# Optimization experiments

Hardware: AMD Instinct MI355X
Metric: run time of the kernel (lower is better)

Reference implementation:

```python
import jax, jax.numpy as jnp
import numpy as np

N_NODES = 50000
N_EDGES = 400000
IN_DIM = 128
HID_DIM = 128
OUT_DIM = 128


def setup_inputs() -> dict:
    key = jax.random.key(0)
    k_x, k_e, k_w1, k_b1, k_w2, k_b2 = jax.random.split(key, 6)
    x = jax.random.normal(k_x, (N_NODES, IN_DIM), dtype=jnp.float32)
    edge_index = jax.random.randint(k_e, (2, N_EDGES), 0, N_NODES, dtype=jnp.int64)
    # nn.Linear-style params: W is [out, in], kaiming-uniform-ish init
    lim1 = 1.0 / np.sqrt(IN_DIM)
    lim2 = 1.0 / np.sqrt(HID_DIM)
    W1 = jax.random.uniform(k_w1, (HID_DIM, IN_DIM), jnp.float32, -lim1, lim1)
    b1 = jax.random.uniform(k_b1, (HID_DIM,), jnp.float32, -lim1, lim1)
    W2 = jax.random.uniform(k_w2, (OUT_DIM, HID_DIM), jnp.float32, -lim2, lim2)
    b2 = jax.random.uniform(k_b2, (OUT_DIM,), jnp.float32, -lim2, lim2)
    return {"x": x, "edge_index": edge_index, "W1": W1, "b1": b1, "W2": W2, "b2": b2}


def reference(x, edge_index, W1, b1, W2, b2):
    # h = relu(fc1(x));  dropout in eval mode -> identity
    h = jax.nn.relu(x @ W1.T + b1)                      # [N, hid]
    src, dst = edge_index[0], edge_index[1]
    # gather messages from src, scatter-add (mean) into dst
    agg = jax.ops.segment_sum(h[src], dst, num_segments=N_NODES)      # [N, hid]
    deg = jax.ops.segment_sum(jnp.ones_like(dst, dtype=h.dtype), dst,
                              num_segments=N_NODES)                   # [N]
    deg = jnp.maximum(deg, 1.0)
    agg = agg / deg[:, None]
    # residual add + fc2
    return (agg + h) @ W2.T + b2                        # [N, out]
```

## Files before the change

kernel.cpp:

```cpp
#include <hip/hip_runtime.h>

#define N_NODES 50000
#define N_EDGES 400000
#define DIM 128
#define N_SCAN_BLK ((N_NODES + 255) / 256)
#define CNT_BLK ((N_EDGES + 1023) / 1024)
#define FC1_BLK ((N_NODES + 63) / 64)
#define AGG_BLK (N_NODES / 16)
#define PADDED_E (N_EDGES + 3 * N_NODES)

typedef unsigned short u16;
typedef unsigned int   u32;
typedef __bf16 v8bf  __attribute__((ext_vector_type(8)));
typedef float  f32x4 __attribute__((ext_vector_type(4)));
typedef u16    u16x8 __attribute__((ext_vector_type(8)));

union BF8 { u16x8 u; v8bf b; };

__device__ __forceinline__ float bf2f(u16 u) {
    union { u32 i; float f; } v; v.i = ((u32)u) << 16; return v.f;
}
__device__ __forceinline__ u16 f2bf(float f) {
    union { float f; u32 i; } v; v.f = f; u32 u = v.i;
    return (u16)((u + 0x7FFFu + ((u >> 16) & 1u)) >> 16);
}

__global__ __launch_bounds__(256, 3) void count_cast_fc1_kernel(
    const int* __restrict__ esrc, const int* __restrict__ edst,
    int* __restrict__ counts, int* __restrict__ occ,
    const float* __restrict__ W2, u16* __restrict__ Wb2,
    const float* __restrict__ x, const float* __restrict__ W1,
    const float* __restrict__ b1, u16* __restrict__ h)
{
    __shared__ u16 xs[64 * 136];
    const int bid = blockIdx.x;

    if (bid < CNT_BLK) {
        int e0 = bid * 1024 + threadIdx.x * 4;
        if (e0 < N_EDGES) {
            int4 d4 = *(const int4*)(edst + e0);
            int4 o;
            o.x = atomicAdd(&counts[d4.x], 1);
            o.y = atomicAdd(&counts[d4.y], 1);
            o.z = atomicAdd(&counts[d4.z], 1);
            o.w = atomicAdd(&counts[d4.w], 1);
            *(int4*)(occ + e0) = o;
        }
        return;
    }
    if (bid < CNT_BLK + 64) {
        int i = (bid - CNT_BLK) * 256 + threadIdx.x;
        Wb2[i] = f2bf(W2[i]);
        return;
    }
    if (bid == CNT_BLK + 64) {
        if (threadIdx.x < 128)
            *(u32*)(h + (size_t)N_NODES * DIM + threadIdx.x * 2) = 0u;
        return;
    }

    const int t = threadIdx.x;
    const int wave = t >> 6, lane = t & 63, quad = lane >> 4, l15 = lane & 15;
    const int ch = wave >> 1, rh = wave & 1;
    const int row0 = (bid - (CNT_BLK + 65)) * 64;

    BF8 barr[4][4];
#pragma unroll
    for (int ct = 0; ct < 4; ++ct)
#pragma unroll
        for (int ks = 0; ks < 4; ++ks) {
            const float* wp = W1 + (size_t)(ch * 64 + ct * 16 + l15) * DIM
                                 + ks * 32 + quad * 8;
            float4 f0 = *(const float4*)wp;
            float4 f1 = *(const float4*)(wp + 4);
            u16x8 p;
            p[0] = f2bf(f0.x); p[1] = f2bf(f0.y); p[2] = f2bf(f0.z); p[3] = f2bf(f0.w);
            p[4] = f2bf(f1.x); p[5] = f2bf(f1.y); p[6] = f2bf(f1.z); p[7] = f2bf(f1.w);
            barr[ct][ks].u = p;
        }

    {
        int srow = t >> 2, k0 = (t & 3) * 32;
        int grow = row0 + srow; if (grow >= N_NODES) grow = N_NODES - 1;
        const float* xp = x + (size_t)grow * DIM + k0;
#pragma unroll
        for (int j = 0; j < 4; ++j) {
            float4 f0 = *(const float4*)(xp + j * 8);
            float4 f1 = *(const float4*)(xp + j * 8 + 4);
            u16x8 p;
            p[0] = f2bf(f0.x); p[1] = f2bf(f0.y); p[2] = f2bf(f0.z); p[3] = f2bf(f0.w);
            p[4] = f2bf(f1.x); p[5] = f2bf(f1.y); p[6] = f2bf(f1.z); p[7] = f2bf(f1.w);
            *(u16x8*)&xs[srow * 136 + k0 + j * 8] = p;
        }
    }

    f32x4 acc[2][4];
#pragma unroll
    for (int ct = 0; ct < 4; ++ct) {
        float bv = b1[ch * 64 + ct * 16 + l15];
        acc[0][ct] = (f32x4){bv, bv, bv, bv};
        acc[1][ct] = (f32x4){bv, bv, bv, bv};
    }
    __syncthreads();

#pragma unroll
    for (int ks = 0; ks < 4; ++ks) {
        BF8 a0, a1;
        a0.u = *(const u16x8*)&xs[(rh * 32 +  0 + l15) * 136 + ks * 32 + quad * 8];
        a1.u = *(const u16x8*)&xs[(rh * 32 + 16 + l15) * 136 + ks * 32 + quad * 8];
#pragma unroll
        for (int ct = 0; ct < 4; ++ct) {
            acc[0][ct] = __builtin_amdgcn_mfma_f32_16x16x32_bf16(
                a0.b, barr[ct][ks].b, acc[0][ct], 0, 0, 0);
            acc[1][ct] = __builtin_amdgcn_mfma_f32_16x16x32_bf16(
                a1.b, barr[ct][ks].b, acc[1][ct], 0, 0, 0);
        }
    }

#pragma unroll
    for (int rt = 0; rt < 2; ++rt)
#pragma unroll
        for (int i = 0; i < 4; ++i) {
            int row = row0 + rh * 32 + rt * 16 + quad * 4 + i;
            if (row < N_NODES) {
#pragma unroll
                for (int ct = 0; ct < 4; ++ct) {
                    int col = ch * 64 + ct * 16 + l15;
                    h[(size_t)row * DIM + col] = f2bf(fmaxf(acc[rt][ct][i], 0.f));
                }
            }
        }
}

__global__ __launch_bounds__(256) void scan_ticket_kernel(
    const int* __restrict__ counts, int* __restrict__ row_ptr,
    int* __restrict__ gcursor, int* __restrict__ esorted)
{
    __shared__ int tmp[256];
    __shared__ int sbase;
    const int t = threadIdx.x;
    const int i = blockIdx.x * 256 + t;
    int deg = (i < N_NODES) ? counts[i] : 0;
    int p = (deg + 3) & ~3;
    tmp[t] = p;
    __syncthreads();
#pragma unroll
    for (int ofs = 1; ofs < 256; ofs <<= 1) {
        int add = (t >= ofs) ? tmp[t - ofs] : 0;
        __syncthreads();
        tmp[t] += add;
        __syncthreads();
    }
    if (t == 255) sbase = atomicAdd(gcursor, tmp[255]);
    __syncthreads();
    if (i < N_NODES) {
        int r = sbase + tmp[t] - p;
        row_ptr[i] = r;
        for (int k = deg; k < p; ++k) esorted[r + k] = N_NODES;
    }
}

__global__ __launch_bounds__(256) void scatter_kernel(
    const int* __restrict__ esrc, const int* __restrict__ edst,
    const int* __restrict__ occ, const int* __restrict__ row_ptr,
    int* __restrict__ esorted)
{
    int e0 = blockIdx.x * 1024 + threadIdx.x * 4;
    if (e0 >= N_EDGES) return;
    int4 s4 = *(const int4*)(esrc + e0);
    int4 d4 = *(const int4*)(edst + e0);
    int4 o4 = *(const int4*)(occ + e0);
    esorted[row_ptr[d4.x] + o4.x] = s4.x;
    esorted[row_ptr[d4.y] + o4.y] = s4.y;
    esorted[row_ptr[d4.z] + o4.z] = s4.z;
    esorted[row_ptr[d4.w] + o4.w] = s4.w;
}

__global__ __launch_bounds__(256) void agg_fc2_kernel(
    const int* __restrict__ row_ptr, const int* __restrict__ counts,
    const int* __restrict__ esorted, const u16* __restrict__ h,
    const u16* __restrict__ Wb2, const float* __restrict__ b2,
    float* __restrict__ out)
{
    __shared__ u16 xs[16 * 136];
    const int t = threadIdx.x;
    const int wv = t >> 6, lane = t & 63, quad = lane >> 4, l15 = lane & 15;
    const int row0 = blockIdx.x * 16;

    {
        const int s = wv * 4 + quad;
        const int n = row0 + s;
        const int start = row_ptr[n];
        const int deg   = counts[n];
        const int plen  = (deg + 3) & ~3;

        u16x8 hres = *(const u16x8*)(h + (size_t)n * DIM + l15 * 8);

        float a[8];
#pragma unroll
        for (int j = 0; j < 8; ++j) a[j] = 0.f;

        const int* ep = esorted + start;
        int k = 0;
        for (; k + 8 <= plen; k += 8) {
            int4 ia = *(const int4*)(ep + k);
            int4 ib = *(const int4*)(ep + k + 4);
            u16x8 v0 = *(const u16x8*)(h + (size_t)ia.x * DIM + l15 * 8);
            u16x8 v1 = *(const u16x8*)(h + (size_t)ia.y * DIM + l15 * 8);
            u16x8 v2 = *(const u16x8*)(h + (size_t)ia.z * DIM + l15 * 8);
            u16x8 v3 = *(const u16x8*)(h + (size_t)ia.w * DIM + l15 * 8);
            u16x8 v4 = *(const u16x8*)(h + (size_t)ib.x * DIM + l15 * 8);
            u16x8 v5 = *(const u16x8*)(h + (size_t)ib.y * DIM + l15 * 8);
            u16x8 v6 = *(const u16x8*)(h + (size_t)ib.z * DIM + l15 * 8);
            u16x8 v7 = *(const u16x8*)(h + (size_t)ib.w * DIM + l15 * 8);
#pragma unroll
            for (int j = 0; j < 8; ++j) {
                a[j] += bf2f(v0[j]); a[j] += bf2f(v1[j]);
                a[j] += bf2f(v2[j]); a[j] += bf2f(v3[j]);
                a[j] += bf2f(v4[j]); a[j] += bf2f(v5[j]);
                a[j] += bf2f(v6[j]); a[j] += bf2f(v7[j]);
            }
        }
        if (k < plen) {
            int4 ia = *(const int4*)(ep + k);
            u16x8 v0 = *(const u16x8*)(h + (size_t)ia.x * DIM + l15 * 8);
            u16x8 v1 = *(const u16x8*)(h + (size_t)ia.y * DIM + l15 * 8);
            u16x8 v2 = *(const u16x8*)(h + (size_t)ia.z * DIM + l15 * 8);
            u16x8 v3 = *(const u16x8*)(h + (size_t)ia.w * DIM + l15 * 8);
#pragma unroll
            for (int j = 0; j < 8; ++j) {
                a[j] += bf2f(v0[j]); a[j] += bf2f(v1[j]);
                a[j] += bf2f(v2[j]); a[j] += bf2f(v3[j]);
            }
        }

        float inv = (deg > 0) ? 1.f / (float)deg : 1.f;
        u16x8 pk;
#pragma unroll
        for (int j = 0; j < 8; ++j)
            pk[j] = f2bf(a[j] * inv + bf2f(hres[j]));
        *(u16x8*)&xs[s * 136 + l15 * 8] = pk;
    }

    BF8 barr[2][4];
#pragma unroll
    for (int ct = 0; ct < 2; ++ct)
#pragma unroll
        for (int ks = 0; ks < 4; ++ks)
            barr[ct][ks].u = *(const u16x8*)(
                Wb2 + (size_t)(wv * 32 + ct * 16 + l15) * DIM + ks * 32 + quad * 8);

    f32x4 acc[2];
#pragma unroll
    for (int ct = 0; ct < 2; ++ct) {
        float bv = b2[wv * 32 + ct * 16 + l15];
        acc[ct] = (f32x4){bv, bv, bv, bv};
    }
    __syncthreads();

#pragma unroll
    for (int ks = 0; ks < 4; ++ks) {
        BF8 a0;
        a0.u = *(const u16x8*)&xs[l15 * 136 + ks * 32 + quad * 8];
#pragma unroll
        for (int ct = 0; ct < 2; ++ct) {
            acc[ct] = __builtin_amdgcn_mfma_f32_16x16x32_bf16(
                a0.b, barr[ct][ks].b, acc[ct], 0, 0, 0);
        }
    }

#pragma unroll
    for (int i = 0; i < 4; ++i) {
        int row = row0 + quad * 4 + i;
#pragma unroll
        for (int ct = 0; ct < 2; ++ct) {
            int col = wv * 32 + ct * 16 + l15;
            out[(size_t)row * DIM + col] = acc[ct][i];
        }
    }
}

extern "C" void kernel_launch(void* const* d_in, const int* in_sizes, int n_in,
                              void* d_out, int out_size, void* d_ws, size_t ws_size,
                              hipStream_t stream)
{
    const float* x  = (const float*)d_in[0];
    const int*   ei = (const int*)d_in[1];
    const float* W1 = (const float*)d_in[2];
    const float* b1 = (const float*)d_in[3];
    const float* W2 = (const float*)d_in[4];
    const float* b2 = (const float*)d_in[5];
    float* out = (float*)d_out;

    const int* esrc = ei;
    const int* edst = ei + N_EDGES;

    char* ws = (char*)d_ws;
    size_t off = 0;
    u16* h       = (u16*)(ws + off); off += (size_t)(N_NODES + 1) * DIM * 2;
    u16* Wb2     = (u16*)(ws + off); off += (size_t)DIM * DIM * 2;
    int* counts  = (int*)(ws + off); off += (size_t)N_NODES * 4;
    int* gcursor = (int*)(ws + off); off += 4;
    int* row_ptr = (int*)(ws + off); off += (size_t)N_NODES * 4;
    int* occ     = (int*)(ws + off); off += (size_t)N_EDGES * 4;
    int* esorted = (int*)(ws + off); off += (size_t)PADDED_E * 4;

    hipMemsetAsync(counts, 0, (size_t)(N_NODES + 1) * 4, stream);

    count_cast_fc1_kernel<<<CNT_BLK + 65 + FC1_BLK, 256, 0, stream>>>(
        esrc, edst, counts, occ, W2, Wb2, x, W1, b1, h);
    scan_ticket_kernel<<<N_SCAN_BLK, 256, 0, stream>>>(
        counts, row_ptr, gcursor, esorted);
    scatter_kernel<<<CNT_BLK, 256, 0, stream>>>(
        esrc, edst, occ, row_ptr, esorted);
    agg_fc2_kernel<<<AGG_BLK, 256, 0, stream>>>(
        row_ptr, counts, esorted, h, Wb2, b2, out);
}
```

Measured before the change: 161.2 us.

## Process two nodes per quad in aggregation and double edges per thread

The aggregation+fc2 kernel now handles 32 nodes per block, with each 16-lane quad gathering two destination rows at once in an interleaved loop. This gives more independent loads in flight, and each wave's W2 fragments feed two MFMA row tiles. The count and scatter passes process 8 edges per thread instead of 4, halving their block counts. The cost is higher register pressure (the launch bound is set to 6 blocks), fewer blocks in the aggregation grid, and possible imbalance when the two paired nodes have very different degrees.

```diff
diff --git a/kernel.cpp b/kernel.cpp
--- a/kernel.cpp
+++ b/kernel.cpp
@@ -4,9 +4,9 @@
 #define N_EDGES 400000
 #define DIM 128
 #define N_SCAN_BLK ((N_NODES + 255) / 256)
-#define CNT_BLK ((N_EDGES + 1023) / 1024)
+#define CNT_BLK ((N_EDGES + 2047) / 2048)
 #define FC1_BLK ((N_NODES + 63) / 64)
-#define AGG_BLK (N_NODES / 16)
+#define AGG_BLK ((N_NODES + 31) / 32)
 #define PADDED_E (N_EDGES + 3 * N_NODES)
 
 typedef unsigned short u16;
@@ -36,15 +36,24 @@
     const int bid = blockIdx.x;
 
     if (bid < CNT_BLK) {
-        int e0 = bid * 1024 + threadIdx.x * 4;
-        if (e0 < N_EDGES) {
-            int4 d4 = *(const int4*)(edst + e0);
-            int4 o;
-            o.x = atomicAdd(&counts[d4.x], 1);
-            o.y = atomicAdd(&counts[d4.y], 1);
-            o.z = atomicAdd(&counts[d4.z], 1);
-            o.w = atomicAdd(&counts[d4.w], 1);
-            *(int4*)(occ + e0) = o;
+        int e0 = bid * 2048 + threadIdx.x * 8;
+        if (e0 + 8 <= N_EDGES) {
+            int4 da = *(const int4*)(edst + e0);
+            int4 db = *(const int4*)(edst + e0 + 4);
+            int4 oa, ob;
+            oa.x = atomicAdd(&counts[da.x], 1);
+            oa.y = atomicAdd(&counts[da.y], 1);
+            oa.z = atomicAdd(&counts[da.z], 1);
+            oa.w = atomicAdd(&counts[da.w], 1);
+            ob.x = atomicAdd(&counts[db.x], 1);
+            ob.y = atomicAdd(&counts[db.y], 1);
+            ob.z = atomicAdd(&counts[db.z], 1);
+            ob.w = atomicAdd(&counts[db.w], 1);
+            *(int4*)(occ + e0)     = oa;
+            *(int4*)(occ + e0 + 4) = ob;
+        } else if (e0 < N_EDGES) {
+            for (int j = 0; j < 8 && e0 + j < N_EDGES; ++j)
+                occ[e0 + j] = atomicAdd(&counts[edst[e0 + j]], 1);
         }
         return;
     }
@@ -165,46 +174,86 @@
     const int* __restrict__ occ, const int* __restrict__ row_ptr,
     int* __restrict__ esorted)
 {
-    int e0 = blockIdx.x * 1024 + threadIdx.x * 4;
-    if (e0 >= N_EDGES) return;
-    int4 s4 = *(const int4*)(esrc + e0);
-    int4 d4 = *(const int4*)(edst + e0);
-    int4 o4 = *(const int4*)(occ + e0);
-    esorted[row_ptr[d4.x] + o4.x] = s4.x;
-    esorted[row_ptr[d4.y] + o4.y] = s4.y;
-    esorted[row_ptr[d4.z] + o4.z] = s4.z;
-    esorted[row_ptr[d4.w] + o4.w] = s4.w;
-}
-
-__global__ __launch_bounds__(256) void agg_fc2_kernel(
+    int e0 = blockIdx.x * 2048 + threadIdx.x * 8;
+    if (e0 + 8 <= N_EDGES) {
+        int4 sa = *(const int4*)(esrc + e0);
+        int4 sb = *(const int4*)(esrc + e0 + 4);
+        int4 da = *(const int4*)(edst + e0);
+        int4 db = *(const int4*)(edst + e0 + 4);
+        int4 oa = *(const int4*)(occ + e0);
+        int4 ob = *(const int4*)(occ + e0 + 4);
+        esorted[row_ptr[da.x] + oa.x] = sa.x;
+        esorted[row_ptr[da.y] + oa.y] = sa.y;
+        esorted[row_ptr[da.z] + oa.z] = sa.z;
+        esorted[row_ptr[da.w] + oa.w] = sa.w;
+        esorted[row_ptr[db.x] + ob.x] = sb.x;
+        esorted[row_ptr[db.y] + ob.y] = sb.y;
+        esorted[row_ptr[db.z] + ob.z] = sb.z;
+        esorted[row_ptr[db.w] + ob.w] = sb.w;
+    } else if (e0 < N_EDGES) {
+        for (int j = 0; j < 8 && e0 + j < N_EDGES; ++j)
+            esorted[row_ptr[edst[e0 + j]] + occ[e0 + j]] = esrc[e0 + j];
+    }
+}
+
+__global__ __launch_bounds__(256, 6) void agg_fc2_kernel(
     const int* __restrict__ row_ptr, const int* __restrict__ counts,
     const int* __restrict__ esorted, const u16* __restrict__ h,
     const u16* __restrict__ Wb2, const float* __restrict__ b2,
     float* __restrict__ out)
 {
-    __shared__ u16 xs[16 * 136];
+    __shared__ u16 xs[32 * 136];
     const int t = threadIdx.x;
     const int wv = t >> 6, lane = t & 63, quad = lane >> 4, l15 = lane & 15;
-    const int row0 = blockIdx.x * 16;
+    const int row0 = blockIdx.x * 32;
 
     {
-        const int s = wv * 4 + quad;
-        const int n = row0 + s;
-        const int start = row_ptr[n];
-        const int deg   = counts[n];
-        const int plen  = (deg + 3) & ~3;
-
-        u16x8 hres = *(const u16x8*)(h + (size_t)n * DIM + l15 * 8);
-
-        float a[8];
-#pragma unroll
-        for (int j = 0; j < 8; ++j) a[j] = 0.f;
-
-        const int* ep = esorted + start;
-        int k = 0;
-        for (; k + 8 <= plen; k += 8) {
-            int4 ia = *(const int4*)(ep + k);
-            int4 ib = *(const int4*)(ep + k + 4);
+        const int s0 = wv * 8 + quad * 2;
+        const int n0 = row0 + s0;
+        const int n1 = n0 + 1;
+        const bool va = (n0 < N_NODES), vb = (n1 < N_NODES);
+        int start0 = 0, deg0 = 0, start1 = 0, deg1 = 0;
+        if (va) { start0 = row_ptr[n0]; deg0 = counts[n0]; }
+        if (vb) { start1 = row_ptr[n1]; deg1 = counts[n1]; }
+        const int plen0 = (deg0 + 3) & ~3;
+        const int plen1 = (deg1 + 3) & ~3;
+
+        u16x8 hres0 = (u16x8){0,0,0,0,0,0,0,0};
+        u16x8 hres1 = (u16x8){0,0,0,0,0,0,0,0};
+        if (va) hres0 = *(const u16x8*)(h + (size_t)n0 * DIM + l15 * 8);
+        if (vb) hres1 = *(const u16x8*)(h + (size_t)n1 * DIM + l15 * 8);
+
+        float a0[8], a1[8];
+#pragma unroll
+        for (int j = 0; j < 8; ++j) { a0[j] = 0.f; a1[j] = 0.f; }
+
+        const int* ep0 = esorted + start0;
+        const int* ep1 = esorted + start1;
+        int k0 = 0, k1 = 0;
+
+        while (k0 < plen0 && k1 < plen1) {
+            int4 ia = *(const int4*)(ep0 + k0);
+            int4 ib = *(const int4*)(ep1 + k1);
+            u16x8 v0 = *(const u16x8*)(h + (size_t)ia.x * DIM + l15 * 8);
+            u16x8 v1 = *(const u16x8*)(h + (size_t)ia.y * DIM + l15 * 8);
+            u16x8 v2 = *(const u16x8*)(h + (size_t)ia.z * DIM + l15 * 8);
+            u16x8 v3 = *(const u16x8*)(h + (size_t)ia.w * DIM + l15 * 8);
+            u16x8 w0 = *(const u16x8*)(h + (size_t)ib.x * DIM + l15 * 8);
+            u16x8 w1 = *(const u16x8*)(h + (size_t)ib.y * DIM + l15 * 8);
+            u16x8 w2 = *(const u16x8*)(h + (size_t)ib.z * DIM + l15 * 8);
+            u16x8 w3 = *(const u16x8*)(h + (size_t)ib.w * DIM + l15 * 8);
+#pragma unroll
+            for (int j = 0; j < 8; ++j) {
+                a0[j] += bf2f(v0[j]); a0[j] += bf2f(v1[j]);
+                a0[j] += bf2f(v2[j]); a0[j] += bf2f(v3[j]);
+                a1[j] += bf2f(w0[j]); a1[j] += bf2f(w1[j]);
+                a1[j] += bf2f(w2[j]); a1[j] += bf2f(w3[j]);
+            }
+            k0 += 4; k1 += 4;
+        }
+        while (k0 + 8 <= plen0) {
+            int4 ia = *(const int4*)(ep0 + k0);
+            int4 ib = *(const int4*)(ep0 + k0 + 4);
             u16x8 v0 = *(const u16x8*)(h + (size_t)ia.x * DIM + l15 * 8);
             u16x8 v1 = *(const u16x8*)(h + (size_t)ia.y * DIM + l15 * 8);
             u16x8 v2 = *(const u16x8*)(h + (size_t)ia.z * DIM + l15 * 8);
@@ -215,31 +264,68 @@
             u16x8 v7 = *(const u16x8*)(h + (size_t)ib.w * DIM + l15 * 8);
 #pragma unroll
             for (int j = 0; j < 8; ++j) {
-                a[j] += bf2f(v0[j]); a[j] += bf2f(v1[j]);
-                a[j] += bf2f(v2[j]); a[j] += bf2f(v3[j]);
-                a[j] += bf2f(v4[j]); a[j] += bf2f(v5[j]);
-                a[j] += bf2f(v6[j]); a[j] += bf2f(v7[j]);
-            }
-        }
-        if (k < plen) {
-            int4 ia = *(const int4*)(ep + k);
+                a0[j] += bf2f(v0[j]); a0[j] += bf2f(v1[j]);
+                a0[j] += bf2f(v2[j]); a0[j] += bf2f(v3[j]);
+                a0[j] += bf2f(v4[j]); a0[j] += bf2f(v5[j]);
+                a0[j] += bf2f(v6[j]); a0[j] += bf2f(v7[j]);
+            }
+            k0 += 8;
+        }
+        if (k0 < plen0) {
+            int4 ia = *(const int4*)(ep0 + k0);
             u16x8 v0 = *(const u16x8*)(h + (size_t)ia.x * DIM + l15 * 8);
             u16x8 v1 = *(const u16x8*)(h + (size_t)ia.y * DIM + l15 * 8);
             u16x8 v2 = *(const u16x8*)(h + (size_t)ia.z * DIM + l15 * 8);
             u16x8 v3 = *(const u16x8*)(h + (size_t)ia.w * DIM + l15 * 8);
 #pragma unroll
             for (int j = 0; j < 8; ++j) {
-                a[j] += bf2f(v0[j]); a[j] += bf2f(v1[j]);
-                a[j] += bf2f(v2[j]); a[j] += bf2f(v3[j]);
-            }
-        }
-
-        float inv = (deg > 0) ? 1.f / (float)deg : 1.f;
-        u16x8 pk;
-#pragma unroll
-        for (int j = 0; j < 8; ++j)
-            pk[j] = f2bf(a[j] * inv + bf2f(hres[j]));
-        *(u16x8*)&xs[s * 136 + l15 * 8] = pk;
+                a0[j] += bf2f(v0[j]); a0[j] += bf2f(v1[j]);
+                a0[j] += bf2f(v2[j]); a0[j] += bf2f(v3[j]);
+            }
+        }
+        while (k1 + 8 <= plen1) {
+            int4 ia = *(const int4*)(ep1 + k1);
+            int4 ib = *(const int4*)(ep1 + k1 + 4);
+            u16x8 v0 = *(const u16x8*)(h + (size_t)ia.x * DIM + l15 * 8);
+            u16x8 v1 = *(const u16x8*)(h + (size_t)ia.y * DIM + l15 * 8);
+            u16x8 v2 = *(const u16x8*)(h + (size_t)ia.z * DIM + l15 * 8);
+            u16x8 v3 = *(const u16x8*)(h + (size_t)ia.w * DIM + l15 * 8);
+            u16x8 v4 = *(const u16x8*)(h + (size_t)ib.x * DIM + l15 * 8);
+            u16x8 v5 = *(const u16x8*)(h + (size_t)ib.y * DIM + l15 * 8);
+            u16x8 v6 = *(const u16x8*)(h + (size_t)ib.z * DIM + l15 * 8);
+            u16x8 v7 = *(const u16x8*)(h + (size_t)ib.w * DIM + l15 * 8);
+#pragma unroll
+            for (int j = 0; j < 8; ++j) {
+                a1[j] += bf2f(v0[j]); a1[j] += bf2f(v1[j]);
+                a1[j] += bf2f(v2[j]); a1[j] += bf2f(v3[j]);
+                a1[j] += bf2f(v4[j]); a1[j] += bf2f(v5[j]);
+                a1[j] += bf2f(v6[j]); a1[j] += bf2f(v7[j]);
+            }
+            k1 += 8;
+        }
+        if (k1 < plen1) {
+            int4 ia = *(const int4*)(ep1 + k1);
+            u16x8 v0 = *(const u16x8*)(h + (size_t)ia.x * DIM + l15 * 8);
+            u16x8 v1 = *(const u16x8*)(h + (size_t)ia.y * DIM + l15 * 8);
+            u16x8 v2 = *(const u16x8*)(h + (size_t)ia.z * DIM + l15 * 8);
+            u16x8 v3 = *(const u16x8*)(h + (size_t)ia.w * DIM + l15 * 8);
+#pragma unroll
+            for (int j = 0; j < 8; ++j) {
+                a1[j] += bf2f(v0[j]); a1[j] += bf2f(v1[j]);
+                a1[j] += bf2f(v2[j]); a1[j] += bf2f(v3[j]);
+            }
+        }
+
+        float inv0 = (deg0 > 0) ? 1.f / (float)deg0 : 1.f;
+        float inv1 = (deg1 > 0) ? 1.f / (float)deg1 : 1.f;
+        u16x8 pk0, pk1;
+#pragma unroll
+        for (int j = 0; j < 8; ++j) {
+            pk0[j] = f2bf(a0[j] * inv0 + bf2f(hres0[j]));
+            pk1[j] = f2bf(a1[j] * inv1 + bf2f(hres1[j]));
+        }
+        *(u16x8*)&xs[s0 * 136 + l15 * 8]       = pk0;
+        *(u16x8*)&xs[(s0 + 1) * 136 + l15 * 8] = pk1;
     }
 
     BF8 barr[2][4];
@@ -250,34 +336,42 @@
             barr[ct][ks].u = *(const u16x8*)(
                 Wb2 + (size_t)(wv * 32 + ct * 16 + l15) * DIM + ks * 32 + quad * 8);
 
-    f32x4 acc[2];
+    f32x4 acc[2][2];
 #pragma unroll
     for (int ct = 0; ct < 2; ++ct) {
         float bv = b2[wv * 32 + ct * 16 + l15];
-        acc[ct] = (f32x4){bv, bv, bv, bv};
+        acc[0][ct] = (f32x4){bv, bv, bv, bv};
+        acc[1][ct] = (f32x4){bv, bv, bv, bv};
     }
     __syncthreads();
 
 #pragma unroll
     for (int ks = 0; ks < 4; ++ks) {
-        BF8 a0;
-        a0.u = *(const u16x8*)&xs[l15 * 136 + ks * 32 + quad * 8];
+        BF8 A0, A1;
+        A0.u = *(const u16x8*)&xs[( 0 + l15) * 136 + ks * 32 + quad * 8];
+        A1.u = *(const u16x8*)&xs[(16 + l15) * 136 + ks * 32 + quad * 8];
 #pragma unroll
         for (int ct = 0; ct < 2; ++ct) {
-            acc[ct] = __builtin_amdgcn_mfma_f32_16x16x32_bf16(
-                a0.b, barr[ct][ks].b, acc[ct], 0, 0, 0);
-        }
-    }
-
-#pragma unroll
-    for (int i = 0; i < 4; ++i) {
-        int row = row0 + quad * 4 + i;
-#pragma unroll
-        for (int ct = 0; ct < 2; ++ct) {
-            int col = wv * 32 + ct * 16 + l15;
-            out[(size_t)row * DIM + col] = acc[ct][i];
-        }
-    }
+            acc[0][ct] = __builtin_amdgcn_mfma_f32_16x16x32_bf16(
+                A0.b, barr[ct][ks].b, acc[0][ct], 0, 0, 0);
+            acc[1][ct] = __builtin_amdgcn_mfma_f32_16x16x32_bf16(
+                A1.b, barr[ct][ks].b, acc[1][ct], 0, 0, 0);
+        }
+    }
+
+#pragma unroll
+    for (int rt = 0; rt < 2; ++rt)
+#pragma unroll
+        for (int i = 0; i < 4; ++i) {
+            int row = row0 + rt * 16 + quad * 4 + i;
+            if (row < N_NODES) {
+#pragma unroll
+                for (int ct = 0; ct < 2; ++ct) {
+                    int col = wv * 32 + ct * 16 + l15;
+                    out[(size_t)row * DIM + col] = acc[rt][ct][i];
+                }
+            }
+        }
 }
 
 extern "C" void kernel_launch(void* const* d_in, const int* in_sizes, int n_in,
```

After: 157.2 us. 2.5% less time.
